# Performance work log

Measured on AMD Instinct MI355X. Metric: run time of the kernel, lower is better.

## Reference

```python
import jax, jax.numpy as jnp
import numpy as np

N = 50000          # nodes
E = 1_600_000      # edges (avg degree 32)
D = 128            # feature dim (in == out)
R = 8              # relation types
LN_EPS = 1e-5


def setup_inputs() -> dict:
    key = jax.random.key(0)
    ks = jax.random.split(key, 6)
    x = jax.random.normal(ks[0], (N, D), dtype=jnp.float32)
    edge_index = jax.random.randint(ks[1], (2, E), 0, N, dtype=jnp.int64)
    edge_type = jax.random.randint(ks[2], (E,), 0, R, dtype=jnp.int64)
    W_rel = jax.random.normal(ks[3], (R, D, D), dtype=jnp.float32) / np.float32(np.sqrt(D))
    W_root = jax.random.normal(ks[4], (D, D), dtype=jnp.float32) / np.float32(np.sqrt(D))
    bias = jnp.zeros((D,), jnp.float32)
    gamma = jnp.ones((D,), jnp.float32)
    beta = jnp.zeros((D,), jnp.float32)
    return dict(x=x, edge_index=edge_index, edge_type=edge_type, node_num=N,
                W_rel=W_rel, W_root=W_root, bias=bias, gamma=gamma, beta=beta)


def reference(x, edge_index, edge_type, node_num, W_rel, W_root, bias, gamma, beta):
    src, dst = edge_index[0], edge_index[1]
    # Relational conv: transform once per relation, then gather per edge.
    xw = jnp.einsum('nd,rdf->rnf', x, W_rel)          # [R, N, D]
    msg = xw[edge_type, src]                           # [E, D]
    # Per-(dst, relation) mean normalization (PyG RGCNConv 'mean' aggr per relation).
    key_idx = dst * R + edge_type                      # [E]
    cnt = jax.ops.segment_sum(jnp.ones((E,), x.dtype), key_idx, num_segments=N * R)
    norm = 1.0 / jnp.maximum(cnt[key_idx], 1.0)        # [E]
    agg = jax.ops.segment_sum(msg * norm[:, None], dst, num_segments=N)  # [N, D]
    feat = agg + x @ W_root + bias                     # self-loop + bias
    feat = feat[:node_num]                             # keep real nodes only
    # norm -> act -> dropout(eval=identity) fusion chain
    mu = jnp.mean(feat, axis=-1, keepdims=True)
    var = jnp.var(feat, axis=-1, keepdims=True)
    feat = (feat - mu) * jax.lax.rsqrt(var + LN_EPS) * gamma + beta
    return jax.nn.relu(feat)
```

## Files before the change

### kernel.cpp

```cpp
#include <hip/hip_runtime.h>
#include <hip/hip_bf16.h>
#include <cstdint>

#define N_NODES 50000
#define N_EDGES 1600000
#define DIM 128
#define NREL 8
#define LN_EPS 1e-5f

#define NKEYS (N_NODES * NREL)
#define PA_BLOCKS ((N_EDGES + 1023) / 1024)
#define NBIN ((NKEYS + 1023) / 1024)
#define BH_STRIDE 1600

#define A_STRIDE 136
#define B_STRIDE 136

#define XB_BLOCKS 6250
#define BT_BLOCKS 576

typedef unsigned short ushort_t;
typedef short short8 __attribute__((ext_vector_type(8)));
typedef float f32x4 __attribute__((ext_vector_type(4)));
typedef unsigned uintx4 __attribute__((ext_vector_type(4)));

__device__ inline ushort_t f2bf(float f) {
    union { float f; unsigned u; } v; v.f = f;
    unsigned r = (v.u + 0x7FFFu + ((v.u >> 16) & 1u)) >> 16;
    return (ushort_t)r;
}
__device__ inline float bf_lo(unsigned u) {
    union { unsigned u; float f; } v; v.u = u << 16;
    return v.f;
}
__device__ inline float bf_hi(unsigned u) {
    union { unsigned u; float f; } v; v.u = u & 0xffff0000u;
    return v.f;
}

__global__ __launch_bounds__(256) void prep_kernel(const float* __restrict__ x,
                                                   ushort_t* __restrict__ xb,
                                                   const float* __restrict__ W_rel,
                                                   const float* __restrict__ W_root,
                                                   ushort_t* __restrict__ Bt,
                                                   const int* __restrict__ ei,
                                                   const int* __restrict__ et,
                                                   unsigned* __restrict__ block_hist) {
    int b = blockIdx.x;
    int tid = threadIdx.x;
    if (b < PA_BLOCKS) {
        __shared__ unsigned hist[NBIN];
        for (int i = tid; i < NBIN; i += 256) hist[i] = 0u;
        __syncthreads();
        int e = b * 1024 + tid;
#pragma unroll
        for (int q = 0; q < 4; ++q) {
            int eq = e + q * 256;
            if (eq < N_EDGES) {
                int dst = ei[N_EDGES + eq];
                unsigned key = (unsigned)dst * NREL + (unsigned)et[eq];
                atomicAdd(&hist[key >> 10], 1u);
            }
        }
        __syncthreads();
        for (int i = tid; i < NBIN; i += 256)
            block_hist[(size_t)i * BH_STRIDE + b] = hist[i];
    } else if (b < PA_BLOCKS + XB_BLOCKS) {
        int i = (b - PA_BLOCKS) * 256 + tid;
        float4 v = ((const float4*)x)[i];
        unsigned lo = (unsigned)f2bf(v.x) | ((unsigned)f2bf(v.y) << 16);
        unsigned hi = (unsigned)f2bf(v.z) | ((unsigned)f2bf(v.w) << 16);
        ((uint2*)xb)[i] = make_uint2(lo, hi);
    } else if (b < PA_BLOCKS + XB_BLOCKS + BT_BLOCKS) {
        int i = (b - PA_BLOCKS - XB_BLOCKS) * 256 + tid;
        int r   = i >> 14;
        int rem = i & 16383;
        int n   = rem >> 7;
        int k   = rem & 127;
        const float* W = (r < NREL) ? (W_rel + (size_t)r * DIM * DIM) : W_root;
        Bt[i] = f2bf(W[(size_t)k * DIM + n]);
    } else {
        if (tid < 32)
            ((uint2*)(xb + (size_t)N_NODES * DIM))[tid] = make_uint2(0u, 0u);
    }
}

__global__ __launch_bounds__(256) void scanA2_kernel(unsigned* __restrict__ bh,
                                                     unsigned* __restrict__ bin_tot) {
    __shared__ unsigned lds[256];
    int k = blockIdx.x;
    int tid = threadIdx.x;
    unsigned* row = bh + (size_t)k * BH_STRIDE;
    int base = tid * 7;
    unsigned v[7];
    unsigned s = 0;
#pragma unroll
    for (int j = 0; j < 7; ++j) {
        int i = base + j;
        v[j] = (i < PA_BLOCKS) ? row[i] : 0u;
        s += v[j];
    }
    lds[tid] = s;
    __syncthreads();
    for (int off = 1; off < 256; off <<= 1) {
        unsigned a = (tid >= off) ? lds[tid - off] : 0u;
        __syncthreads();
        lds[tid] += a;
        __syncthreads();
    }
    unsigned ex = lds[tid] - s;
#pragma unroll
    for (int j = 0; j < 7; ++j) {
        int i = base + j;
        if (i < PA_BLOCKS) {
            unsigned t = v[j];
            row[i] = ex;
            ex += t;
        }
    }
    if (tid == 255) bin_tot[k] = lds[255];
}

__global__ __launch_bounds__(512) void scanA3_kernel(const unsigned* __restrict__ bin_tot,
                                                     unsigned* __restrict__ bin_base) {
    __shared__ unsigned lds[512];
    int tid = threadIdx.x;
    unsigned v = (tid < NBIN) ? bin_tot[tid] : 0u;
    lds[tid] = v;
    __syncthreads();
    for (int off = 1; off < 512; off <<= 1) {
        unsigned a = (tid >= off) ? lds[tid - off] : 0u;
        __syncthreads();
        lds[tid] += a;
        __syncthreads();
    }
    if (tid < NBIN) bin_base[tid] = lds[tid] - v;
}

__global__ __launch_bounds__(256) void passB_kernel(const int* __restrict__ ei,
                                                    const int* __restrict__ et,
                                                    const unsigned* __restrict__ bh,
                                                    const unsigned* __restrict__ bin_base,
                                                    unsigned* __restrict__ rec) {
    __shared__ unsigned col[NBIN];
    __shared__ unsigned rk[NBIN];
    int b = blockIdx.x;
    int tid = threadIdx.x;
    for (int i = tid; i < NBIN; i += 256) {
        col[i] = bin_base[i] + bh[(size_t)i * BH_STRIDE + b];
        rk[i]  = 0u;
    }
    __syncthreads();
    int e = b * 1024 + tid;
#pragma unroll
    for (int q = 0; q < 4; ++q) {
        int eq = e + q * 256;
        if (eq < N_EDGES) {
            int src = ei[eq];
            int dst = ei[N_EDGES + eq];
            unsigned key = (unsigned)dst * NREL + (unsigned)et[eq];
            unsigned bin = key >> 10;
            unsigned r = atomicAdd(&rk[bin], 1u);
            rec[col[bin] + r] = ((unsigned)src << 10) | (key & 1023u);
        }
    }
}

__global__ __launch_bounds__(256) void passC_kernel(const unsigned* __restrict__ rec,
                                                    const unsigned* __restrict__ bin_base,
                                                    const unsigned* __restrict__ bin_tot,
                                                    uint2* __restrict__ meta,
                                                    int* __restrict__ sorted_src) {
    __shared__ unsigned cnt[1024];
    __shared__ unsigned lds[256];
    int k = blockIdx.x;
    int tid = threadIdx.x;
    unsigned base = bin_base[k];
    unsigned tot  = bin_tot[k];
    for (int i = tid; i < 1024; i += 256) cnt[i] = 0u;
    __syncthreads();
    for (unsigned i = tid; i < tot; i += 256) {
        unsigned r = rec[base + i];
        atomicAdd(&cnt[r & 1023u], 1u);
    }
    __syncthreads();
    unsigned v[4], incl[4], s = 0;
#pragma unroll
    for (int j = 0; j < 4; ++j) {
        v[j] = cnt[tid * 4 + j];
        s += v[j];
        incl[j] = s;
    }
    lds[tid] = s;
    __syncthreads();
    for (int off = 1; off < 256; off <<= 1) {
        unsigned a = (tid >= off) ? lds[tid - off] : 0u;
        __syncthreads();
        lds[tid] += a;
        __syncthreads();
    }
    unsigned bs = lds[tid] - s;
    unsigned key0 = (unsigned)k * 1024 + tid * 4;
#pragma unroll
    for (int j = 0; j < 4; ++j) {
        unsigned ex = bs + incl[j] - v[j];
        if (key0 + j < NKEYS) meta[key0 + j] = make_uint2(base + ex, v[j]);
    }
    __syncthreads();
#pragma unroll
    for (int j = 0; j < 4; ++j) cnt[tid * 4 + j] = bs + incl[j] - v[j];
    __syncthreads();
    for (unsigned i = tid; i < tot; i += 256) {
        unsigned r = rec[base + i];
        unsigned q = r & 1023u;
        unsigned p = atomicAdd(&cnt[q], 1u);
        sorted_src[base + p] = (int)(r >> 10);
    }
}

__global__ __launch_bounds__(256) void aggregate_kernel(const uint2* __restrict__ meta,
                                                        const int* __restrict__ sorted_src,
                                                        const ushort_t* __restrict__ xb,
                                                        ushort_t* __restrict__ h,
                                                        int r0, int cr) {
    int hw = threadIdx.x >> 5;
    int sl = threadIdx.x & 31;
    int g0 = blockIdx.x * 16 + hw * 2;
    int g1 = g0 + 1;
    int total = N_NODES * cr;
    if (g0 >= total) return;

    unsigned st0, mc0, st1 = 0u, mc1 = 0u;
    if (cr == NREL) {
        uint4 mm = *(const uint4*)&meta[(unsigned)g0];
        st0 = mm.x; mc0 = mm.y;
        st1 = mm.z; mc1 = mm.w;
    } else {
        int n0 = g0 / cr, rl0 = g0 - n0 * cr;
        unsigned key0 = (unsigned)n0 * NREL + (unsigned)(r0 + rl0);
        uint2 md0 = meta[key0];
        st0 = md0.x; mc0 = md0.y;
        if (g1 < total) {
            int n1 = g1 / cr, rl1 = g1 - n1 * cr;
            unsigned key1 = (unsigned)n1 * NREL + (unsigned)(r0 + rl1);
            uint2 md1 = meta[key1];
            st1 = md1.x; mc1 = md1.y;
        }
    }

    float a00 = 0.f, a01 = 0.f, a02 = 0.f, a03 = 0.f;
    float a10 = 0.f, a11 = 0.f, a12 = 0.f, a13 = 0.f;
    const char* xbase = (const char*)xb;
    unsigned slb = (unsigned)sl << 3;

    unsigned c0 = 0, c1 = 0;
    while (c0 < mc0 || c1 < mc1) {
        int sv0 = (c0 + (unsigned)sl < mc0) ? sorted_src[st0 + c0 + sl] : N_NODES;
        int sv1 = (c1 + (unsigned)sl < mc1) ? sorted_src[st1 + c1 + sl] : N_NODES;
        unsigned rem0 = (c0 < mc0) ? ((mc0 - c0 > 32u) ? 32u : (mc0 - c0)) : 0u;
        unsigned rem1 = (c1 < mc1) ? ((mc1 - c1 > 32u) ? 32u : (mc1 - c1)) : 0u;
        unsigned rm = rem0 > rem1 ? rem0 : rem1;
        for (unsigned j = 0; j < rm; j += 4) {
            int s00 = __shfl(sv0, (int)j,     32);
            int s01 = __shfl(sv0, (int)j + 1, 32);
            int s02 = __shfl(sv0, (int)j + 2, 32);
            int s03 = __shfl(sv0, (int)j + 3, 32);
            int s10 = __shfl(sv1, (int)j,     32);
            int s11 = __shfl(sv1, (int)j + 1, 32);
            int s12 = __shfl(sv1, (int)j + 2, 32);
            int s13 = __shfl(sv1, (int)j + 3, 32);
            uint2 d00 = *(const uint2*)(xbase + ((((unsigned)s00) << 8) | slb));
            uint2 d01 = *(const uint2*)(xbase + ((((unsigned)s01) << 8) | slb));
            uint2 d02 = *(const uint2*)(xbase + ((((unsigned)s02) << 8) | slb));
            uint2 d03 = *(const uint2*)(xbase + ((((unsigned)s03) << 8) | slb));
            uint2 d10 = *(const uint2*)(xbase + ((((unsigned)s10) << 8) | slb));
            uint2 d11 = *(const uint2*)(xbase + ((((unsigned)s11) << 8) | slb));
            uint2 d12 = *(const uint2*)(xbase + ((((unsigned)s12) << 8) | slb));
            uint2 d13 = *(const uint2*)(xbase + ((((unsigned)s13) << 8) | slb));
            a00 += (bf_lo(d00.x) + bf_lo(d01.x)) + (bf_lo(d02.x) + bf_lo(d03.x));
            a01 += (bf_hi(d00.x) + bf_hi(d01.x)) + (bf_hi(d02.x) + bf_hi(d03.x));
            a02 += (bf_lo(d00.y) + bf_lo(d01.y)) + (bf_lo(d02.y) + bf_lo(d03.y));
            a03 += (bf_hi(d00.y) + bf_hi(d01.y)) + (bf_hi(d02.y) + bf_hi(d03.y));
            a10 += (bf_lo(d10.x) + bf_lo(d11.x)) + (bf_lo(d12.x) + bf_lo(d13.x));
            a11 += (bf_hi(d10.x) + bf_hi(d11.x)) + (bf_hi(d12.x) + bf_hi(d13.x));
            a12 += (bf_lo(d10.y) + bf_lo(d11.y)) + (bf_lo(d12.y) + bf_lo(d13.y));
            a13 += (bf_hi(d10.y) + bf_hi(d11.y)) + (bf_hi(d12.y) + bf_hi(d13.y));
        }
        c0 += rem0;
        c1 += rem1;
    }

    float inv0 = 1.0f / fmaxf((float)mc0, 1.0f);
    unsigned lo0 = (unsigned)f2bf(a00 * inv0) | ((unsigned)f2bf(a01 * inv0) << 16);
    unsigned hi0 = (unsigned)f2bf(a02 * inv0) | ((unsigned)f2bf(a03 * inv0) << 16);
    ((uint2*)(h + (size_t)g0 * DIM))[sl] = make_uint2(lo0, hi0);
    if (g1 < total) {
        float inv1 = 1.0f / fmaxf((float)mc1, 1.0f);
        unsigned lo1 = (unsigned)f2bf(a10 * inv1) | ((unsigned)f2bf(a11 * inv1) << 16);
        unsigned hi1 = (unsigned)f2bf(a12 * inv1) | ((unsigned)f2bf(a13 * inv1) << 16);
        ((uint2*)(h + (size_t)g1 * DIM))[sl] = make_uint2(lo1, hi1);
    }
}

__global__ __launch_bounds__(512) void gemm_ln_kernel(const ushort_t* __restrict__ h,
                                                      int cr, int r0,
                                                      const ushort_t* __restrict__ xb,
                                                      const ushort_t* __restrict__ Bt,
                                                      int include_root,
                                                      const float* __restrict__ bias,
                                                      const float* __restrict__ gamma,
                                                      const float* __restrict__ beta,
                                                      float* __restrict__ out,
                                                      int accumulate, int do_ln) {
    __shared__ __align__(16) ushort_t As[128 * A_STRIDE];
    __shared__ __align__(16) ushort_t Bs[128 * B_STRIDE];

    int tid  = threadIdx.x;
    int w    = tid >> 6;
    int lane = tid & 63;
    int m    = lane & 15;
    int quad = lane >> 4;
    int n0   = blockIdx.x * 128;

    f32x4 acc[8];
#pragma unroll
    for (int j = 0; j < 8; ++j) acc[j] = (f32x4){0.f, 0.f, 0.f, 0.f};

    int nrel = cr + include_root;
    for (int rr = 0; rr < nrel; ++rr) {
        int rel = (rr < cr) ? (r0 + rr) : NREL;

#pragma unroll
        for (int p = 0; p < 4; ++p) {
            int c = tid + 512 * p;
            int row = c >> 4, ch = c & 15;
            uintx4 v = *(const uintx4*)(Bt + ((size_t)rel * DIM + row) * DIM + ch * 8);
            *(uintx4*)&Bs[row * B_STRIDE + ch * 8] = v;
        }
#pragma unroll
        for (int p = 0; p < 4; ++p) {
            int c = tid + 512 * p;
            int row = c >> 4, ch = c & 15;
            uintx4 v = (uintx4){0u, 0u, 0u, 0u};
            int node = n0 + row;
            if (node < N_NODES) {
                const ushort_t* src = (rr < cr)
                    ? (h + ((size_t)node * cr + rr) * DIM)
                    : (xb + (size_t)node * DIM);
                v = *(const uintx4*)(src + ch * 8);
            }
            *(uintx4*)&As[row * A_STRIDE + ch * 8] = v;
        }
        __syncthreads();

#pragma unroll
        for (int t = 0; t < 4; ++t) {
            short8 af = *(const short8*)&As[(w * 16 + m) * A_STRIDE + t * 32 + quad * 8];
#pragma unroll
            for (int j = 0; j < 8; ++j) {
                short8 bf = *(const short8*)&Bs[(j * 16 + m) * B_STRIDE + t * 32 + quad * 8];
                acc[j] = __builtin_amdgcn_mfma_f32_16x16x32_bf16(af, bf, acc[j], 0, 0, 0);
            }
        }
        __syncthreads();
    }

    if (do_ln) {
        float bj[8], gj[8], btj[8];
#pragma unroll
        for (int j = 0; j < 8; ++j) {
            bj[j]  = bias[j * 16 + m];
            gj[j]  = gamma[j * 16 + m];
            btj[j] = beta[j * 16 + m];
        }
#pragma unroll
        for (int i = 0; i < 4; ++i) {
            float s = 0.f, sq = 0.f;
#pragma unroll
            for (int j = 0; j < 8; ++j) {
                float v = acc[j][i] + bj[j];
                s  += v;
                sq += v * v;
            }
#pragma unroll
            for (int off = 1; off < 16; off <<= 1) {
                s  += __shfl_xor(s, off, 64);
                sq += __shfl_xor(sq, off, 64);
            }
            float mean = s * (1.0f / DIM);
            float var  = sq * (1.0f / DIM) - mean * mean;
            float rstd = rsqrtf(var + LN_EPS);
            int node = n0 + w * 16 + quad * 4 + i;
            if (node < N_NODES) {
#pragma unroll
                for (int j = 0; j < 8; ++j) {
                    float v = acc[j][i] + bj[j];
                    v = (v - mean) * rstd * gj[j] + btj[j];
                    out[(size_t)node * DIM + j * 16 + m] = fmaxf(v, 0.f);
                }
            }
        }
    } else {
#pragma unroll
        for (int i = 0; i < 4; ++i) {
            int node = n0 + w * 16 + quad * 4 + i;
            if (node < N_NODES) {
#pragma unroll
                for (int j = 0; j < 8; ++j) {
                    size_t o = (size_t)node * DIM + j * 16 + m;
                    float v = acc[j][i];
                    if (accumulate) v += out[o];
                    out[o] = v;
                }
            }
        }
    }
}

__global__ __launch_bounds__(256) void ln_kernel(float* __restrict__ out,
                                                 const float* __restrict__ bias,
                                                 const float* __restrict__ gamma,
                                                 const float* __restrict__ beta) {
    int row  = blockIdx.x * 4 + (threadIdx.x >> 6);
    int lane = threadIdx.x & 63;
    if (row >= N_NODES) return;
    float2 v = *(float2*)(out + (size_t)row * DIM + lane * 2);
    float2 bi = *(const float2*)(bias + lane * 2);
    v.x += bi.x;
    v.y += bi.y;
    float s  = v.x + v.y;
    float sq = v.x * v.x + v.y * v.y;
#pragma unroll
    for (int off = 32; off > 0; off >>= 1) {
        s  += __shfl_xor(s, off, 64);
        sq += __shfl_xor(sq, off, 64);
    }
    float mean = s * (1.0f / DIM);
    float var  = sq * (1.0f / DIM) - mean * mean;
    float rstd = rsqrtf(var + LN_EPS);
    float2 g = *(const float2*)(gamma + lane * 2);
    float2 b = *(const float2*)(beta + lane * 2);
    v.x = fmaxf((v.x - mean) * rstd * g.x + b.x, 0.f);
    v.y = fmaxf((v.y - mean) * rstd * g.y + b.y, 0.f);
    *(float2*)(out + (size_t)row * DIM + lane * 2) = v;
}

extern "C" void kernel_launch(void* const* d_in, const int* in_sizes, int n_in,
                              void* d_out, int out_size, void* d_ws, size_t ws_size,
                              hipStream_t stream) {
    const float* x      = (const float*)d_in[0];
    const int*   ei     = (const int*)d_in[1];
    const int*   et     = (const int*)d_in[2];
    const float* W_rel  = (const float*)d_in[4];
    const float* W_root = (const float*)d_in[5];
    const float* bias   = (const float*)d_in[6];
    const float* gamma  = (const float*)d_in[7];
    const float* beta   = (const float*)d_in[8];
    float*       out    = (float*)d_out;

    char* ws = (char*)d_ws;
    size_t off = 0;
    auto alloc = [&](size_t bytes) { char* p = ws + off; off = (off + bytes + 255) & ~(size_t)255; return p; };
    unsigned* block_hist = (unsigned*)alloc((size_t)NBIN * BH_STRIDE * 4);
    unsigned* bin_tot    = (unsigned*)alloc((size_t)NBIN * 4);
    unsigned* bin_base   = (unsigned*)alloc((size_t)NBIN * 4);
    unsigned* rec        = (unsigned*)alloc((size_t)N_EDGES * 4);
    uint2*    meta       = (uint2*)alloc((size_t)NKEYS * 8);
    int*      sorted_src = (int*)alloc((size_t)N_EDGES * 4);
    ushort_t* Bt         = (ushort_t*)alloc((size_t)9 * DIM * DIM * 2);
    ushort_t* xb         = (ushort_t*)alloc((size_t)(N_NODES + 1) * DIM * 2);
    size_t fixedOff = off;
    ushort_t* h = (ushort_t*)(ws + fixedOff);
    size_t availB = ws_size > fixedOff ? ws_size - fixedOff : 0;
    size_t perRel = (size_t)N_NODES * DIM * 2;
    int chunkR = (int)(availB / perRel);
    if (chunkR > NREL) chunkR = NREL;
    if (chunkR < 1)    chunkR = 1;

    prep_kernel<<<PA_BLOCKS + XB_BLOCKS + BT_BLOCKS + 1, 256, 0, stream>>>(
        x, xb, W_rel, W_root, Bt, ei, et, block_hist);
    scanA2_kernel<<<NBIN, 256, 0, stream>>>(block_hist, bin_tot);
    scanA3_kernel<<<1, 512, 0, stream>>>(bin_tot, bin_base);
    passB_kernel<<<PA_BLOCKS, 256, 0, stream>>>(ei, et, block_hist, bin_base, rec);
    passC_kernel<<<NBIN, 256, 0, stream>>>(rec, bin_base, bin_tot, meta, sorted_src);

    int gemmGrid = (N_NODES + 127) / 128;

    if (chunkR >= NREL) {
        int nbuck = N_NODES * NREL;
        aggregate_kernel<<<(nbuck + 15) / 16, 256, 0, stream>>>(meta, sorted_src,
                                                                xb, h, 0, NREL);
        gemm_ln_kernel<<<gemmGrid, 512, 0, stream>>>(h, NREL, 0, xb, Bt, 1,
                                                     bias, gamma, beta, out, 0, 1);
    } else {
        for (int r0 = 0; r0 < NREL; r0 += chunkR) {
            int cr = (NREL - r0 < chunkR) ? (NREL - r0) : chunkR;
            int nbuck = N_NODES * cr;
            aggregate_kernel<<<(nbuck + 15) / 16, 256, 0, stream>>>(meta, sorted_src,
                                                                    xb, h, r0, cr);
            int include_root = (r0 + cr == NREL) ? 1 : 0;
            gemm_ln_kernel<<<gemmGrid, 512, 0, stream>>>(h, cr, r0, xb, Bt, include_root,
                                                         bias, gamma, beta, out,
                                                         r0 > 0 ? 1 : 0, 0);
        }
        ln_kernel<<<(N_NODES + 3) / 4, 256, 0, stream>>>(out, bias, gamma, beta);
    }
}
```

Baseline: 255.1 us.

## Fuse per-relation neighbor aggregation into GEMM tile load, drop intermediate buffer

Replaces the separate aggregate kernel and chunked GEMM/LN path with a single kernel that gathers and mean-normalizes neighbor features per relation directly into the shared-memory A tile before each relation's MFMA step. This removes writing and re-reading the large bf16 per-relation aggregate buffer and extra launches. In exchange, the latency-bound gather now runs in a grid of only a few hundred 512-thread blocks with no overlap between gather and matrix math, which may hurt latency hiding.

```diff
diff --git a/kernel.cpp b/kernel.cpp
--- a/kernel.cpp
+++ b/kernel.cpp
@@ -218,100 +218,14 @@
     }
 }
 
-__global__ __launch_bounds__(256) void aggregate_kernel(const uint2* __restrict__ meta,
-                                                        const int* __restrict__ sorted_src,
-                                                        const ushort_t* __restrict__ xb,
-                                                        ushort_t* __restrict__ h,
-                                                        int r0, int cr) {
-    int hw = threadIdx.x >> 5;
-    int sl = threadIdx.x & 31;
-    int g0 = blockIdx.x * 16 + hw * 2;
-    int g1 = g0 + 1;
-    int total = N_NODES * cr;
-    if (g0 >= total) return;
-
-    unsigned st0, mc0, st1 = 0u, mc1 = 0u;
-    if (cr == NREL) {
-        uint4 mm = *(const uint4*)&meta[(unsigned)g0];
-        st0 = mm.x; mc0 = mm.y;
-        st1 = mm.z; mc1 = mm.w;
-    } else {
-        int n0 = g0 / cr, rl0 = g0 - n0 * cr;
-        unsigned key0 = (unsigned)n0 * NREL + (unsigned)(r0 + rl0);
-        uint2 md0 = meta[key0];
-        st0 = md0.x; mc0 = md0.y;
-        if (g1 < total) {
-            int n1 = g1 / cr, rl1 = g1 - n1 * cr;
-            unsigned key1 = (unsigned)n1 * NREL + (unsigned)(r0 + rl1);
-            uint2 md1 = meta[key1];
-            st1 = md1.x; mc1 = md1.y;
-        }
-    }
-
-    float a00 = 0.f, a01 = 0.f, a02 = 0.f, a03 = 0.f;
-    float a10 = 0.f, a11 = 0.f, a12 = 0.f, a13 = 0.f;
-    const char* xbase = (const char*)xb;
-    unsigned slb = (unsigned)sl << 3;
-
-    unsigned c0 = 0, c1 = 0;
-    while (c0 < mc0 || c1 < mc1) {
-        int sv0 = (c0 + (unsigned)sl < mc0) ? sorted_src[st0 + c0 + sl] : N_NODES;
-        int sv1 = (c1 + (unsigned)sl < mc1) ? sorted_src[st1 + c1 + sl] : N_NODES;
-        unsigned rem0 = (c0 < mc0) ? ((mc0 - c0 > 32u) ? 32u : (mc0 - c0)) : 0u;
-        unsigned rem1 = (c1 < mc1) ? ((mc1 - c1 > 32u) ? 32u : (mc1 - c1)) : 0u;
-        unsigned rm = rem0 > rem1 ? rem0 : rem1;
-        for (unsigned j = 0; j < rm; j += 4) {
-            int s00 = __shfl(sv0, (int)j,     32);
-            int s01 = __shfl(sv0, (int)j + 1, 32);
-            int s02 = __shfl(sv0, (int)j + 2, 32);
-            int s03 = __shfl(sv0, (int)j + 3, 32);
-            int s10 = __shfl(sv1, (int)j,     32);
-            int s11 = __shfl(sv1, (int)j + 1, 32);
-            int s12 = __shfl(sv1, (int)j + 2, 32);
-            int s13 = __shfl(sv1, (int)j + 3, 32);
-            uint2 d00 = *(const uint2*)(xbase + ((((unsigned)s00) << 8) | slb));
-            uint2 d01 = *(const uint2*)(xbase + ((((unsigned)s01) << 8) | slb));
-            uint2 d02 = *(const uint2*)(xbase + ((((unsigned)s02) << 8) | slb));
-            uint2 d03 = *(const uint2*)(xbase + ((((unsigned)s03) << 8) | slb));
-            uint2 d10 = *(const uint2*)(xbase + ((((unsigned)s10) << 8) | slb));
-            uint2 d11 = *(const uint2*)(xbase + ((((unsigned)s11) << 8) | slb));
-            uint2 d12 = *(const uint2*)(xbase + ((((unsigned)s12) << 8) | slb));
-            uint2 d13 = *(const uint2*)(xbase + ((((unsigned)s13) << 8) | slb));
-            a00 += (bf_lo(d00.x) + bf_lo(d01.x)) + (bf_lo(d02.x) + bf_lo(d03.x));
-            a01 += (bf_hi(d00.x) + bf_hi(d01.x)) + (bf_hi(d02.x) + bf_hi(d03.x));
-            a02 += (bf_lo(d00.y) + bf_lo(d01.y)) + (bf_lo(d02.y) + bf_lo(d03.y));
-            a03 += (bf_hi(d00.y) + bf_hi(d01.y)) + (bf_hi(d02.y) + bf_hi(d03.y));
-            a10 += (bf_lo(d10.x) + bf_lo(d11.x)) + (bf_lo(d12.x) + bf_lo(d13.x));
-            a11 += (bf_hi(d10.x) + bf_hi(d11.x)) + (bf_hi(d12.x) + bf_hi(d13.x));
-            a12 += (bf_lo(d10.y) + bf_lo(d11.y)) + (bf_lo(d12.y) + bf_lo(d13.y));
-            a13 += (bf_hi(d10.y) + bf_hi(d11.y)) + (bf_hi(d12.y) + bf_hi(d13.y));
-        }
-        c0 += rem0;
-        c1 += rem1;
-    }
-
-    float inv0 = 1.0f / fmaxf((float)mc0, 1.0f);
-    unsigned lo0 = (unsigned)f2bf(a00 * inv0) | ((unsigned)f2bf(a01 * inv0) << 16);
-    unsigned hi0 = (unsigned)f2bf(a02 * inv0) | ((unsigned)f2bf(a03 * inv0) << 16);
-    ((uint2*)(h + (size_t)g0 * DIM))[sl] = make_uint2(lo0, hi0);
-    if (g1 < total) {
-        float inv1 = 1.0f / fmaxf((float)mc1, 1.0f);
-        unsigned lo1 = (unsigned)f2bf(a10 * inv1) | ((unsigned)f2bf(a11 * inv1) << 16);
-        unsigned hi1 = (unsigned)f2bf(a12 * inv1) | ((unsigned)f2bf(a13 * inv1) << 16);
-        ((uint2*)(h + (size_t)g1 * DIM))[sl] = make_uint2(lo1, hi1);
-    }
-}
-
-__global__ __launch_bounds__(512) void gemm_ln_kernel(const ushort_t* __restrict__ h,
-                                                      int cr, int r0,
-                                                      const ushort_t* __restrict__ xb,
-                                                      const ushort_t* __restrict__ Bt,
-                                                      int include_root,
-                                                      const float* __restrict__ bias,
-                                                      const float* __restrict__ gamma,
-                                                      const float* __restrict__ beta,
-                                                      float* __restrict__ out,
-                                                      int accumulate, int do_ln) {
+__global__ __launch_bounds__(512, 4) void gemm_fused_kernel(const uint2* __restrict__ meta,
+                                                            const int* __restrict__ sorted_src,
+                                                            const ushort_t* __restrict__ xb,
+                                                            const ushort_t* __restrict__ Bt,
+                                                            const float* __restrict__ bias,
+                                                            const float* __restrict__ gamma,
+                                                            const float* __restrict__ beta,
+                                                            float* __restrict__ out) {
     __shared__ __align__(16) ushort_t As[128 * A_STRIDE];
     __shared__ __align__(16) ushort_t Bs[128 * B_STRIDE];
 
@@ -320,36 +234,105 @@
     int lane = tid & 63;
     int m    = lane & 15;
     int quad = lane >> 4;
+    int hw   = tid >> 5;
+    int sl   = tid & 31;
+    unsigned slb = (unsigned)sl << 3;
     int n0   = blockIdx.x * 128;
+    const char* xbase = (const char*)xb;
+
+    int rowc[4], chc[4];
+#pragma unroll
+    for (int p = 0; p < 4; ++p) {
+        int c = tid + 512 * p;
+        rowc[p] = c >> 4;
+        chc[p]  = c & 15;
+    }
 
     f32x4 acc[8];
 #pragma unroll
     for (int j = 0; j < 8; ++j) acc[j] = (f32x4){0.f, 0.f, 0.f, 0.f};
 
-    int nrel = cr + include_root;
-    for (int rr = 0; rr < nrel; ++rr) {
-        int rel = (rr < cr) ? (r0 + rr) : NREL;
-
+    for (int rr = 0; rr <= NREL; ++rr) {
 #pragma unroll
         for (int p = 0; p < 4; ++p) {
-            int c = tid + 512 * p;
-            int row = c >> 4, ch = c & 15;
-            uintx4 v = *(const uintx4*)(Bt + ((size_t)rel * DIM + row) * DIM + ch * 8);
-            *(uintx4*)&Bs[row * B_STRIDE + ch * 8] = v;
-        }
-#pragma unroll
-        for (int p = 0; p < 4; ++p) {
-            int c = tid + 512 * p;
-            int row = c >> 4, ch = c & 15;
-            uintx4 v = (uintx4){0u, 0u, 0u, 0u};
-            int node = n0 + row;
-            if (node < N_NODES) {
-                const ushort_t* src = (rr < cr)
-                    ? (h + ((size_t)node * cr + rr) * DIM)
-                    : (xb + (size_t)node * DIM);
-                v = *(const uintx4*)(src + ch * 8);
+            uintx4 v = *(const uintx4*)(Bt + ((size_t)rr * DIM + rowc[p]) * DIM + chc[p] * 8);
+            *(uintx4*)&Bs[rowc[p] * B_STRIDE + chc[p] * 8] = v;
+        }
+
+        if (rr < NREL) {
+#pragma unroll
+            for (int p = 0; p < 4; ++p) {
+                int row0 = hw * 8 + p * 2;
+                int row1 = row0 + 1;
+                int nd0  = n0 + row0;
+                int nd1  = n0 + row1;
+                unsigned st0 = 0u, mc0 = 0u, st1 = 0u, mc1 = 0u;
+                if (nd0 < N_NODES) {
+                    uint2 md = meta[(unsigned)nd0 * NREL + (unsigned)rr];
+                    st0 = md.x; mc0 = md.y;
+                }
+                if (nd1 < N_NODES) {
+                    uint2 md = meta[(unsigned)nd1 * NREL + (unsigned)rr];
+                    st1 = md.x; mc1 = md.y;
+                }
+
+                float a00 = 0.f, a01 = 0.f, a02 = 0.f, a03 = 0.f;
+                float a10 = 0.f, a11 = 0.f, a12 = 0.f, a13 = 0.f;
+                unsigned c0 = 0, c1 = 0;
+                while (c0 < mc0 || c1 < mc1) {
+                    int sv0 = (c0 + (unsigned)sl < mc0) ? sorted_src[st0 + c0 + sl] : N_NODES;
+                    int sv1 = (c1 + (unsigned)sl < mc1) ? sorted_src[st1 + c1 + sl] : N_NODES;
+                    unsigned rem0 = (c0 < mc0) ? ((mc0 - c0 > 32u) ? 32u : (mc0 - c0)) : 0u;
+                    unsigned rem1 = (c1 < mc1) ? ((mc1 - c1 > 32u) ? 32u : (mc1 - c1)) : 0u;
+                    unsigned rm = rem0 > rem1 ? rem0 : rem1;
+                    for (unsigned j = 0; j < rm; j += 4) {
+                        int s00 = __shfl(sv0, (int)j,     32);
+                        int s01 = __shfl(sv0, (int)j + 1, 32);
+                        int s02 = __shfl(sv0, (int)j + 2, 32);
+                        int s03 = __shfl(sv0, (int)j + 3, 32);
+                        int s10 = __shfl(sv1, (int)j,     32);
+                        int s11 = __shfl(sv1, (int)j + 1, 32);
+                        int s12 = __shfl(sv1, (int)j + 2, 32);
+                        int s13 = __shfl(sv1, (int)j + 3, 32);
+                        uint2 d00 = *(const uint2*)(xbase + ((((unsigned)s00) << 8) | slb));
+                        uint2 d01 = *(const uint2*)(xbase + ((((unsigned)s01) << 8) | slb));
+                        uint2 d02 = *(const uint2*)(xbase + ((((unsigned)s02) << 8) | slb));
+                        uint2 d03 = *(const uint2*)(xbase + ((((unsigned)s03) << 8) | slb));
+                        uint2 d10 = *(const uint2*)(xbase + ((((unsigned)s10) << 8) | slb));
+                        uint2 d11 = *(const uint2*)(xbase + ((((unsigned)s11) << 8) | slb));
+                        uint2 d12 = *(const uint2*)(xbase + ((((unsigned)s12) << 8) | slb));
+                        uint2 d13 = *(const uint2*)(xbase + ((((unsigned)s13) << 8) | slb));
+                        a00 += (bf_lo(d00.x) + bf_lo(d01.x)) + (bf_lo(d02.x) + bf_lo(d03.x));
+                        a01 += (bf_hi(d00.x) + bf_hi(d01.x)) + (bf_hi(d02.x) + bf_hi(d03.x));
+                        a02 += (bf_lo(d00.y) + bf_lo(d01.y)) + (bf_lo(d02.y) + bf_lo(d03.y));
+                        a03 += (bf_hi(d00.y) + bf_hi(d01.y)) + (bf_hi(d02.y) + bf_hi(d03.y));
+                        a10 += (bf_lo(d10.x) + bf_lo(d11.x)) + (bf_lo(d12.x) + bf_lo(d13.x));
+                        a11 += (bf_hi(d10.x) + bf_hi(d11.x)) + (bf_hi(d12.x) + bf_hi(d13.x));
+                        a12 += (bf_lo(d10.y) + bf_lo(d11.y)) + (bf_lo(d12.y) + bf_lo(d13.y));
+                        a13 += (bf_hi(d10.y) + bf_hi(d11.y)) + (bf_hi(d12.y) + bf_hi(d13.y));
+                    }
+                    c0 += rem0;
+                    c1 += rem1;
+                }
+
+                float inv0 = 1.0f / fmaxf((float)mc0, 1.0f);
+                unsigned lo0 = (unsigned)f2bf(a00 * inv0) | ((unsigned)f2bf(a01 * inv0) << 16);
+                unsigned hi0 = (unsigned)f2bf(a02 * inv0) | ((unsigned)f2bf(a03 * inv0) << 16);
+                *(uint2*)&As[row0 * A_STRIDE + sl * 4] = make_uint2(lo0, hi0);
+                float inv1 = 1.0f / fmaxf((float)mc1, 1.0f);
+                unsigned lo1 = (unsigned)f2bf(a10 * inv1) | ((unsigned)f2bf(a11 * inv1) << 16);
+                unsigned hi1 = (unsigned)f2bf(a12 * inv1) | ((unsigned)f2bf(a13 * inv1) << 16);
+                *(uint2*)&As[row1 * A_STRIDE + sl * 4] = make_uint2(lo1, hi1);
             }
-            *(uintx4*)&As[row * A_STRIDE + ch * 8] = v;
+        } else {
+#pragma unroll
+            for (int p = 0; p < 4; ++p) {
+                uintx4 v = (uintx4){0u, 0u, 0u, 0u};
+                int node = n0 + rowc[p];
+                if (node < N_NODES)
+                    v = *(const uintx4*)(xb + (size_t)node * DIM + chc[p] * 8);
+                *(uintx4*)&As[rowc[p] * A_STRIDE + chc[p] * 8] = v;
+            }
         }
         __syncthreads();
 
@@ -365,84 +348,40 @@
         __syncthreads();
     }
 
-    if (do_ln) {
-        float bj[8], gj[8], btj[8];
+    float bj[8], gj[8], btj[8];
+#pragma unroll
+    for (int j = 0; j < 8; ++j) {
+        bj[j]  = bias[j * 16 + m];
+        gj[j]  = gamma[j * 16 + m];
+        btj[j] = beta[j * 16 + m];
+    }
+#pragma unroll
+    for (int i = 0; i < 4; ++i) {
+        float s = 0.f, sq = 0.f;
 #pragma unroll
         for (int j = 0; j < 8; ++j) {
-            bj[j]  = bias[j * 16 + m];
-            gj[j]  = gamma[j * 16 + m];
-            btj[j] = beta[j * 16 + m];
-        }
-#pragma unroll
-        for (int i = 0; i < 4; ++i) {
-            float s = 0.f, sq = 0.f;
+            float v = acc[j][i] + bj[j];
+            s  += v;
+            sq += v * v;
+        }
+#pragma unroll
+        for (int off = 1; off < 16; off <<= 1) {
+            s  += __shfl_xor(s, off, 64);
+            sq += __shfl_xor(sq, off, 64);
+        }
+        float mean = s * (1.0f / DIM);
+        float var  = sq * (1.0f / DIM) - mean * mean;
+        float rstd = rsqrtf(var + LN_EPS);
+        int node = n0 + w * 16 + quad * 4 + i;
+        if (node < N_NODES) {
 #pragma unroll
             for (int j = 0; j < 8; ++j) {
                 float v = acc[j][i] + bj[j];
-                s  += v;
-                sq += v * v;
+                v = (v - mean) * rstd * gj[j] + btj[j];
+                out[(size_t)node * DIM + j * 16 + m] = fmaxf(v, 0.f);
             }
-#pragma unroll
-            for (int off = 1; off < 16; off <<= 1) {
-                s  += __shfl_xor(s, off, 64);
-                sq += __shfl_xor(sq, off, 64);
-            }
-            float mean = s * (1.0f / DIM);
-            float var  = sq * (1.0f / DIM) - mean * mean;
-            float rstd = rsqrtf(var + LN_EPS);
-            int node = n0 + w * 16 + quad * 4 + i;
-            if (node < N_NODES) {
-#pragma unroll
-                for (int j = 0; j < 8; ++j) {
-                    float v = acc[j][i] + bj[j];
-                    v = (v - mean) * rstd * gj[j] + btj[j];
-                    out[(size_t)node * DIM + j * 16 + m] = fmaxf(v, 0.f);
-                }
-            }
-        }
-    } else {
-#pragma unroll
-        for (int i = 0; i < 4; ++i) {
-            int node = n0 + w * 16 + quad * 4 + i;
-            if (node < N_NODES) {
-#pragma unroll
-                for (int j = 0; j < 8; ++j) {
-                    size_t o = (size_t)node * DIM + j * 16 + m;
-                    float v = acc[j][i];
-                    if (accumulate) v += out[o];
-                    out[o] = v;
-                }
-            }
-        }
-    }
-}
-
-__global__ __launch_bounds__(256) void ln_kernel(float* __restrict__ out,
-                                                 const float* __restrict__ bias,
-                                                 const float* __restrict__ gamma,
-                                                 const float* __restrict__ beta) {
-    int row  = blockIdx.x * 4 + (threadIdx.x >> 6);
-    int lane = threadIdx.x & 63;
-    if (row >= N_NODES) return;
-    float2 v = *(float2*)(out + (size_t)row * DIM + lane * 2);
-    float2 bi = *(const float2*)(bias + lane * 2);
-    v.x += bi.x;
-    v.y += bi.y;
-    float s  = v.x + v.y;
-    float sq = v.x * v.x + v.y * v.y;
-#pragma unroll
-    for (int off = 32; off > 0; off >>= 1) {
-        s  += __shfl_xor(s, off, 64);
-        sq += __shfl_xor(sq, off, 64);
-    }
-    float mean = s * (1.0f / DIM);
-    float var  = sq * (1.0f / DIM) - mean * mean;
-    float rstd = rsqrtf(var + LN_EPS);
-    float2 g = *(const float2*)(gamma + lane * 2);
-    float2 b = *(const float2*)(beta + lane * 2);
-    v.x = fmaxf((v.x - mean) * rstd * g.x + b.x, 0.f);
-    v.y = fmaxf((v.y - mean) * rstd * g.y + b.y, 0.f);
-    *(float2*)(out + (size_t)row * DIM + lane * 2) = v;
+        }
+    }
 }
 
 extern "C" void kernel_launch(void* const* d_in, const int* in_sizes, int n_in,
@@ -469,13 +408,7 @@
     int*      sorted_src = (int*)alloc((size_t)N_EDGES * 4);
     ushort_t* Bt         = (ushort_t*)alloc((size_t)9 * DIM * DIM * 2);
     ushort_t* xb         = (ushort_t*)alloc((size_t)(N_NODES + 1) * DIM * 2);
-    size_t fixedOff = off;
-    ushort_t* h = (ushort_t*)(ws + fixedOff);
-    size_t availB = ws_size > fixedOff ? ws_size - fixedOff : 0;
-    size_t perRel = (size_t)N_NODES * DIM * 2;
-    int chunkR = (int)(availB / perRel);
-    if (chunkR > NREL) chunkR = NREL;
-    if (chunkR < 1)    chunkR = 1;
+    (void)ws_size;
 
     prep_kernel<<<PA_BLOCKS + XB_BLOCKS + BT_BLOCKS + 1, 256, 0, stream>>>(
         x, xb, W_rel, W_root, Bt, ei, et, block_hist);
@@ -485,24 +418,6 @@
     passC_kernel<<<NBIN, 256, 0, stream>>>(rec, bin_base, bin_tot, meta, sorted_src);
 
     int gemmGrid = (N_NODES + 127) / 128;
-
-    if (chunkR >= NREL) {
-        int nbuck = N_NODES * NREL;
-        aggregate_kernel<<<(nbuck + 15) / 16, 256, 0, stream>>>(meta, sorted_src,
-                                                                xb, h, 0, NREL);
-        gemm_ln_kernel<<<gemmGrid, 512, 0, stream>>>(h, NREL, 0, xb, Bt, 1,
-                                                     bias, gamma, beta, out, 0, 1);
-    } else {
-        for (int r0 = 0; r0 < NREL; r0 += chunkR) {
-            int cr = (NREL - r0 < chunkR) ? (NREL - r0) : chunkR;
-            int nbuck = N_NODES * cr;
-            aggregate_kernel<<<(nbuck + 15) / 16, 256, 0, stream>>>(meta, sorted_src,
-                                                                    xb, h, r0, cr);
-            int include_root = (r0 + cr == NREL) ? 1 : 0;
-            gemm_ln_kernel<<<gemmGrid, 512, 0, stream>>>(h, cr, r0, xb, Bt, include_root,
-                                                         bias, gamma, beta, out,
-                                                         r0 > 0 ? 1 : 0, 0);
-        }
-        ln_kernel<<<(N_NODES + 3) / 4, 256, 0, stream>>>(out, bias, gamma, beta);
-    }
-}
+    gemm_fused_kernel<<<gemmGrid, 512, 0, stream>>>(meta, sorted_src, xb, Bt,
+                                                    bias, gamma, beta, out);
+}
```

After: 286.6 us. 1.12x slower.
